# Performance work log

Hardware: AMD Instinct MI355X
Metric: run time of the kernel (lower is better)

Reference implementation:

```python
import jax, jax.numpy as jnp
import numpy as np

KS = 3
N = KS ** 3  # 27 kernel sample points


def conv3d(x, w, b=None, pad=1):
    out = jax.lax.conv_general_dilated(
        x, w, (1, 1, 1), [(pad, pad)] * 3,
        dimension_numbers=('NCDHW', 'OIDHW', 'NCDHW'))
    if b is not None:
        out = out + b[None, :, None, None, None]
    return out


def batchnorm(x, g, b, eps=1e-5):
    # training-mode BN: batch statistics over (N,D,H,W), biased variance (torch default)
    m = x.mean(axis=(0, 2, 3, 4), keepdims=True)
    v = x.var(axis=(0, 2, 3, 4), keepdims=True)
    return (x - m) * jax.lax.rsqrt(v + eps) * g[None, :, None, None, None] + b[None, :, None, None, None]


def deform_conv3d(x, offset, w, pad=1):
    # x: (b,c,D,H,W); offset: (b,3N,D,H,W) channel order [d-offsets | h-offsets | w-offsets]
    b, c, D, H, W = x.shape
    xp = jnp.pad(x, ((0, 0), (0, 0), (pad, pad), (pad, pad), (pad, pad)))
    Dp, Hp, Wp = D + 2 * pad, H + 2 * pad, W + 2 * pad
    dt = offset.dtype
    r = (jnp.arange(KS) - (KS - 1) // 2).astype(dt)
    pn = jnp.stack(jnp.meshgrid(r, r, r, indexing='ij'), -1).reshape(N, 3)  # kernel grid offsets
    base = jnp.stack(jnp.meshgrid(jnp.arange(D) + pad, jnp.arange(H) + pad,
                                  jnp.arange(W) + pad, indexing='ij'), -1).astype(dt)  # (D,H,W,3)
    off = jnp.transpose(offset.reshape(b, 3, N, D, H, W), (0, 3, 4, 5, 2, 1))  # (b,D,H,W,N,3)
    p = base[None, :, :, :, None, :] + pn[None, None, None, None] + off  # fractional sample coords
    dims = jnp.array([Dp, Hp, Wp], dtype=dt)
    q0 = jnp.floor(p)
    q0c = jnp.clip(q0, 0, dims - 1)
    q1c = jnp.clip(q0 + 1, 0, dims - 1)
    pc = jnp.clip(p, 0, dims - 1)
    wlo = 1.0 + (q0c - pc)  # per-axis trilinear weight, low corner
    whi = 1.0 - (q1c - pc)  # per-axis trilinear weight, high corner
    q0i = q0c.astype(jnp.int32)
    q1i = q1c.astype(jnp.int32)
    xpf = xp.reshape(b, c, -1)
    M = D * H * W * N
    acc = jnp.zeros((b, c, D, H, W, N), dtype=x.dtype)
    for corner in range(8):  # fixed 8 trilinear corners
        sel = [(corner >> a) & 1 for a in range(3)]
        q = [q1i[..., a] if sel[a] else q0i[..., a] for a in range(3)]
        g = (whi[..., 0] if sel[0] else wlo[..., 0]) \
            * (whi[..., 1] if sel[1] else wlo[..., 1]) \
            * (whi[..., 2] if sel[2] else wlo[..., 2])
        idx = (q[0] * Hp + q[1]) * Wp + q[2]  # (b,D,H,W,N) flat gather index
        vals = jnp.take_along_axis(
            xpf, jnp.broadcast_to(idx.reshape(b, 1, M), (b, c, M)), axis=2
        ).reshape(b, c, D, H, W, N)
        acc = acc + g[:, None] * vals
    # kernel-stride-KS conv over the reshaped blocks == contraction over (c, N)
    outc = w.shape[0]
    return jnp.einsum('bcdhwn,ocn->bodhw', acc, w.reshape(outc, c, N))


def setup_inputs():
    key = jax.random.key(0)
    ks = jax.random.split(key, 8)
    f32 = jnp.float32
    return {
        'x': jax.random.normal(ks[0], (16, 1, 28, 28, 28), f32),
        'off_w': jax.random.normal(ks[1], (81, 1, 3, 3, 3), f32) * 0.05,
        'off_b': jnp.zeros((81,), f32),
        'dconv_w': jax.random.normal(ks[2], (32, 1, 3, 3, 3), f32) * 0.2,
        'bn1_g': jnp.ones((32,), f32), 'bn1_b': jnp.zeros((32,), f32),
        'conv2_w': jax.random.normal(ks[3], (64, 32, 3, 3, 3), f32) * 0.06,
        'conv2_b': jnp.zeros((64,), f32),
        'bn2_g': jnp.ones((64,), f32), 'bn2_b': jnp.zeros((64,), f32),
        'conv3_w': jax.random.normal(ks[4], (128, 64, 3, 3, 3), f32) * 0.04,
        'conv3_b': jnp.zeros((128,), f32),
        'bn3_g': jnp.ones((128,), f32), 'bn3_b': jnp.zeros((128,), f32),
        'conv4_w': jax.random.normal(ks[5], (128, 128, 3, 3, 3), f32) * 0.03,
        'conv4_b': jnp.zeros((128,), f32),
        'bn4_g': jnp.ones((128,), f32), 'bn4_b': jnp.zeros((128,), f32),
        'fc_w': jax.random.normal(ks[6], (10, 128), f32) * 0.1,
        'fc_b': jnp.zeros((10,), f32),
    }


def reference(x, off_w, off_b, dconv_w, bn1_g, bn1_b, conv2_w, conv2_b, bn2_g, bn2_b,
              conv3_w, conv3_b, bn3_g, bn3_b, conv4_w, conv4_b, bn4_g, bn4_b, fc_w, fc_b):
    offsets = conv3d(x, off_w, off_b)  # (b,81,D,H,W)
    h = batchnorm(jax.nn.relu(deform_conv3d(x, offsets, dconv_w)), bn1_g, bn1_b)
    h = batchnorm(jax.nn.relu(conv3d(h, conv2_w, conv2_b)), bn2_g, bn2_b)
    h = batchnorm(jax.nn.relu(conv3d(h, conv3_w, conv3_b)), bn3_g, bn3_b)
    h = batchnorm(jax.nn.relu(conv3d(h, conv4_w, conv4_b)), bn4_g, bn4_b)
    h = h.mean(axis=(2, 3, 4))  # avg_pool3d over full (28,28,d) -> (b,128)
    logits = h @ fc_w.T + fc_b
    return jax.nn.log_softmax(logits, axis=1), offsets
```

## Files before the change

kernel.cpp:

```cpp
#include <hip/hip_runtime.h>
#include <math.h>

#define Sv 21952
#define HWc 784
#define CNT 351232.0f
#define EPS 1e-5f
#define PV 27000
#define PT (16 * PV)

typedef short bf16x8 __attribute__((ext_vector_type(8)));
typedef float f32x4 __attribute__((ext_vector_type(4)));
typedef float f32x16 __attribute__((ext_vector_type(16)));
typedef unsigned short u16x8 __attribute__((ext_vector_type(8)));

__device__ __forceinline__ unsigned short f2bf(float f) {
    unsigned u = __float_as_uint(f);
    u = (u + 0x7FFFu + ((u >> 16) & 1u)) >> 16;
    return (unsigned short)u;
}
__device__ __forceinline__ float bf2f(unsigned short h) {
    return __uint_as_float(((unsigned)h) << 16);
}

__device__ __forceinline__ void async16(const unsigned short* g, unsigned short* l) {
    __builtin_amdgcn_global_load_lds(
        (const __attribute__((address_space(1))) unsigned int*)g,
        (__attribute__((address_space(3))) unsigned int*)l, 16, 0, 0);
}

template<int C>
__global__ __launch_bounds__(256) void k_zborder(unsigned short* __restrict__ buf) {
    int idx = blockIdx.x * 256 + threadIdx.x;
    if (idx >= PT) return;
    int p = idx % PV;
    int z = p / 900, y = (p / 30) % 30, x = p % 30;
    if (z >= 1 && z <= 28 && y >= 1 && y <= 28 && x >= 1 && x <= 28) return;
    u16x8 zv = {0, 0, 0, 0, 0, 0, 0, 0};
    u16x8* dst = (u16x8*)(buf + (long)idx * C);
    #pragma unroll
    for (int q = 0; q < C / 8; q++) dst[q] = zv;
}

__global__ __launch_bounds__(256) void k_offsets(const float* __restrict__ x,
        const float* __restrict__ ow, const float* __restrict__ ob,
        float* __restrict__ out) {
    int idx = blockIdx.x * 256 + threadIdx.x;
    int n = idx / Sv, s = idx % Sv;
    int d = s / HWc, r = s % HWc, h = r / 28, w = r % 28;
    const float* xb = x + (long)n * Sv;
    float xv[27];
    #pragma unroll
    for (int dz = 0; dz < 3; dz++)
      #pragma unroll
      for (int dy = 0; dy < 3; dy++)
        #pragma unroll
        for (int dx = 0; dx < 3; dx++) {
            int zz = d + dz - 1, yy = h + dy - 1, xx = w + dx - 1;
            bool ok = (unsigned)zz < 28u && (unsigned)yy < 28u && (unsigned)xx < 28u;
            xv[dz * 9 + dy * 3 + dx] = ok ? xb[zz * HWc + yy * 28 + xx] : 0.f;
        }
    float* op = out + (long)n * 81 * Sv + s;
    for (int c = 0; c < 81; c++) {
        float acc = ob[c];
        #pragma unroll
        for (int k = 0; k < 27; k++) acc += xv[k] * ow[c * 27 + k];
        op[(long)c * Sv] = acc;
    }
}

__device__ __forceinline__ float fetch_pad(const float* __restrict__ xb,
                                           int zq, int yq, int xq) {
    int z = zq - 1, y = yq - 1, xx = xq - 1;
    bool ok = (unsigned)z < 28u && (unsigned)y < 28u && (unsigned)xx < 28u;
    return ok ? xb[z * HWc + y * 28 + xx] : 0.f;
}

__global__ __launch_bounds__(256) void k_deform(const float* __restrict__ x,
        const float* __restrict__ off, const float* __restrict__ dw,
        unsigned short* __restrict__ h1p) {
    __shared__ float w_s[32 * 27];
    for (int i = threadIdx.x; i < 32 * 27; i += 256) w_s[i] = dw[i];
    __syncthreads();
    int idx = blockIdx.x * 256 + threadIdx.x;
    int n = idx / Sv, s = idx % Sv;
    int d = s / HWc, r = s % HWc, h = r / 28, w = r % 28;
    const float* xb = x + (long)n * Sv;
    const float* ofb = off + (long)n * 81 * Sv + s;
    float v[27];
    #pragma unroll
    for (int k = 0; k < 27; k++) {
        int ki = k / 9, kj = (k / 3) % 3, kl = k % 3;
        float pd = (float)(d + ki) + ofb[(long)k * Sv];
        float ph = (float)(h + kj) + ofb[(long)(27 + k) * Sv];
        float pw = (float)(w + kl) + ofb[(long)(54 + k) * Sv];
        float q0d = floorf(pd), q0h = floorf(ph), q0w = floorf(pw);
        float pcd = fminf(fmaxf(pd, 0.f), 29.f);
        float pch = fminf(fmaxf(ph, 0.f), 29.f);
        float pcw = fminf(fmaxf(pw, 0.f), 29.f);
        float q0cd = fminf(fmaxf(q0d, 0.f), 29.f);
        float q0ch = fminf(fmaxf(q0h, 0.f), 29.f);
        float q0cw = fminf(fmaxf(q0w, 0.f), 29.f);
        float q1cd = fminf(fmaxf(q0d + 1.f, 0.f), 29.f);
        float q1ch = fminf(fmaxf(q0h + 1.f, 0.f), 29.f);
        float q1cw = fminf(fmaxf(q0w + 1.f, 0.f), 29.f);
        float wz[2] = {1.f + (q0cd - pcd), 1.f - (q1cd - pcd)};
        float wy[2] = {1.f + (q0ch - pch), 1.f - (q1ch - pch)};
        float wx[2] = {1.f + (q0cw - pcw), 1.f - (q1cw - pcw)};
        int qz[2] = {(int)q0cd, (int)q1cd};
        int qy[2] = {(int)q0ch, (int)q1ch};
        int qx[2] = {(int)q0cw, (int)q1cw};
        float val = 0.f;
        #pragma unroll
        for (int cz = 0; cz < 2; cz++)
          #pragma unroll
          for (int cy = 0; cy < 2; cy++)
            #pragma unroll
            for (int cx = 0; cx < 2; cx++)
                val += wz[cz] * wy[cy] * wx[cx] * fetch_pad(xb, qz[cz], qy[cy], qx[cx]);
        v[k] = val;
    }
    unsigned pb = ((((unsigned)n * 30 + (d + 1)) * 30 + (h + 1)) * 30 + (w + 1)) * 32;
    unsigned short tmp[32];
    #pragma unroll
    for (int o = 0; o < 32; o++) {
        float acc = 0.f;
        #pragma unroll
        for (int k = 0; k < 27; k++) acc += v[k] * w_s[o * 27 + k];
        tmp[o] = f2bf(fmaxf(acc, 0.f));
    }
    u16x8* dst = (u16x8*)(h1p + pb);
    #pragma unroll
    for (int q = 0; q < 4; q++) dst[q] = ((u16x8*)tmp)[q];
}

template<int C>
__global__ __launch_bounds__(256) void k_stats_p(const unsigned short* __restrict__ buf,
        float* __restrict__ sums) {
    constexpr int G = C / 8;
    constexpr int P = 256 / G;
    int t = threadIdx.x;
    int oct = t % G, ps = t / G;
    float s1[8], s2[8];
    #pragma unroll
    for (int j = 0; j < 8; j++) { s1[j] = 0.f; s2[j] = 0.f; }
    for (int p = blockIdx.x * P + ps; p < PT; p += gridDim.x * P) {
        u16x8 v = *(const u16x8*)(buf + (long)p * C + oct * 8);
        #pragma unroll
        for (int j = 0; j < 8; j++) {
            float f = bf2f(v[j]);
            s1[j] += f; s2[j] += f * f;
        }
    }
    __shared__ float sh[2][C];
    if (t < C) { sh[0][t] = 0.f; sh[1][t] = 0.f; }
    __syncthreads();
    #pragma unroll
    for (int j = 0; j < 8; j++) {
        atomicAdd(&sh[0][oct * 8 + j], s1[j]);
        atomicAdd(&sh[1][oct * 8 + j], s2[j]);
    }
    __syncthreads();
    if (t < C) { atomicAdd(&sums[t], sh[0][t]); atomicAdd(&sums[C + t], sh[1][t]); }
}

__global__ void k_finalize(const float* __restrict__ sums, const float* __restrict__ g,
        const float* __restrict__ bb, float* __restrict__ aff, int C) {
    int c = threadIdx.x;
    if (c < C) {
        float mean = sums[c] * (1.f / CNT);
        float var = sums[C + c] * (1.f / CNT) - mean * mean;
        float a = g[c] * rsqrtf(var + EPS);
        aff[c] = a;
        aff[C + c] = bb[c] - mean * a;
    }
}

template<int CI, int COT>
__global__ __launch_bounds__(256) void k_wfrag32(const float* __restrict__ w,
        const float* __restrict__ affa, unsigned short* __restrict__ wf) {
    constexpr int NT32 = COT / 32;
    constexpr int KC = CI / 32;
    int tid = blockIdx.x * 256 + threadIdx.x;
    int lane = tid & 63, rest = tid >> 6;
    int kh = rest & 1; rest >>= 1;
    int nt = rest % NT32; rest /= NT32;
    int kc = rest % KC;
    int tap = rest / KC;
    if (tap >= 27) return;
    int co = nt * 32 + (lane & 31);
    int hi = lane >> 5;
    unsigned short tmp[8];
    #pragma unroll
    for (int j = 0; j < 8; j++) {
        int ci = kc * 32 + kh * 16 + hi * 8 + j;
        tmp[j] = f2bf(w[((long)co * CI + ci) * 27 + tap] * affa[ci]);
    }
    long oidx = ((((long)kc * 27 + tap) * NT32 + nt) * 2 + kh) * 512 + lane * 8;
    *(u16x8*)(wf + oidx) = *(u16x8*)tmp;
}

template<int CI, int COT>
__global__ __launch_bounds__(256) void k_tapsum(const float* __restrict__ w,
        const float* __restrict__ affb, float* __restrict__ S) {
    __shared__ float acc[27];
    int co = blockIdx.x;
    int t = threadIdx.x;
    if (t < 27) acc[t] = 0.f;
    __syncthreads();
    const float* wr = w + (long)co * CI * 27;
    for (int idx = t; idx < CI * 27; idx += 256)
        atomicAdd(&acc[idx % 27], wr[idx] * affb[idx / 27]);
    __syncthreads();
    if (t < 27) S[t * COT + co] = acc[t];
}

template<int COT>
__global__ void k_btab2(const float* __restrict__ S, const float* __restrict__ bias,
        float* __restrict__ T) {
    int tid = blockIdx.x * 256 + threadIdx.x;
    if (tid >= 27 * COT) return;
    int co = tid % COT, cls = tid / COT;
    int xc = cls % 3, yc = (cls / 3) % 3, zc = cls / 9;
    float val = bias[co];
    #pragma unroll
    for (int t = 0; t < 27; t++) {
        int dx = t % 3, dy = (t / 3) % 3, dz = t / 9;
        bool ok = (zc == 1 || (zc == 0 && dz >= 1) || (zc == 2 && dz <= 1))
               && (yc == 1 || (yc == 0 && dy >= 1) || (yc == 2 && dy <= 1))
               && (xc == 1 || (xc == 0 && dx >= 1) || (xc == 2 && dx <= 1));
        if (ok) val += S[t * COT + co];
    }
    T[cls * COT + co] = val;
}

template<int CI, int COT, int WN, bool PAD_OUT, int SMODE>
__global__ __launch_bounds__(WN * 128, 2) void k_conv_mfma(
        const unsigned short* __restrict__ in,
        const unsigned short* __restrict__ wfrag,
        const float* __restrict__ Ttab,
        unsigned short* __restrict__ out,
        float* __restrict__ sa, float* __restrict__ sb) {
    constexpr int KC = CI / 32;
    constexpr int NT32 = COT / 32;
    constexpr int NTW = NT32 / 2;
    constexpr int NT = WN * 128;
    constexpr int CP = 720;
    constexpr int CUU = CP * 5;
    constexpr int NLOAD = (CUU + NT - 1) / NT;
    constexpr int LDSU = CUU + 48;
    __shared__ unsigned short lds[LDSU * 8];
    __shared__ float shs[2][COT];

    int tid = threadIdx.x, wv = tid >> 6, lane = tid & 63;
    int lcol = lane & 31, hi = lane >> 5;
    int wv_m = wv & 1, wv_n = wv >> 1;
    if (tid < COT) { shs[0][tid] = 0.f; shs[1][tid] = 0.f; }

    int bx = blockIdx.x;
    int xcd = bx & 7, loc = bx >> 3;
    int n = xcd * 2 + loc / 98;
    int rem = loc % 98;
    int z0 = (rem / 7) * 2;
    int y0 = (rem % 7) * 4;
    const unsigned short* src = in + ((long)((n * 30 + z0) * 30 + y0) * 30) * CI;

    int baseA[4];
    #pragma unroll
    for (int mt = 0; mt < 4; mt++) {
        int x = lcol; if (x > 27) x = 27;
        int pos = (wv_m * 6 + mt) * 30 + x;
        baseA[mt] = pos * 80 + hi * 16;
    }

    f32x16 acc[4][NTW];
    #pragma unroll
    for (int mt = 0; mt < 4; mt++)
        #pragma unroll
        for (int nt = 0; nt < NTW; nt++)
            #pragma unroll
            for (int e = 0; e < 16; e++) acc[mt][nt][e] = 0.f;

    for (int kc = 0; kc < KC; kc++) {
        if (kc) __syncthreads();
        #pragma unroll
        for (int j = 0; j < NLOAD; j++) {
            int wb = j * NT + (wv << 6);
            if (wb < CUU) {
                int u = wb + lane;
                if (u >= CUU) u = CUU - 1;
                int p = u / 5, s = u - p * 5;
                int q = s & 3;
                int zl = p / 180, r = p - zl * 180;
                int yl = r / 30, xl = r - yl * 30;
                int so = (zl * 900 + yl * 30 + xl) * CI + q * 8 + kc * 32;
                async16(src + so, lds + (wb << 3));
            }
        }
        __syncthreads();
        const unsigned short* pwk =
            wfrag + (long)(kc * 27) * NT32 * 1024 + (long)wv_n * (NTW * 1024)
                  + lane * 8;
        bf16x8 bc[NTW][2];
        #pragma unroll
        for (int nt = 0; nt < NTW; nt++)
            #pragma unroll
            for (int kh = 0; kh < 2; kh++)
                bc[nt][kh] = *(const bf16x8*)(pwk + nt * 1024 + kh * 512);
        #pragma unroll
        for (int tap = 0; tap < 27; tap++) {
            int td = (((tap / 9) * 6 + (tap % 9) / 3) * 30 + tap % 3) * 80;
            bf16x8 bn[NTW][2];
            if (tap < 26) {
                const unsigned short* pwn = pwk + (long)(tap + 1) * NT32 * 1024;
                #pragma unroll
                for (int nt = 0; nt < NTW; nt++)
                    #pragma unroll
                    for (int kh = 0; kh < 2; kh++)
                        bn[nt][kh] = *(const bf16x8*)(pwn + nt * 1024 + kh * 512);
            }
            bf16x8 a[2][4];
            #pragma unroll
            for (int kh = 0; kh < 2; kh++)
                #pragma unroll
                for (int mt = 0; mt < 4; mt++)
                    a[kh][mt] = *(const bf16x8*)((const char*)lds
                                 + baseA[mt] + td + kh * 32);
            #pragma unroll
            for (int kh = 0; kh < 2; kh++)
                #pragma unroll
                for (int mt = 0; mt < 4; mt++)
                    #pragma unroll
                    for (int nt = 0; nt < NTW; nt++)
                        acc[mt][nt] = __builtin_amdgcn_mfma_f32_32x32x16_bf16(
                            a[kh][mt], bc[nt][kh], acc[mt][nt], 0, 0, 0);
            if (tap < 26) {
                #pragma unroll
                for (int nt = 0; nt < NTW; nt++)
                    #pragma unroll
                    for (int kh = 0; kh < 2; kh++)
                        bc[nt][kh] = bn[nt][kh];
            }
        }
    }

    int zz = z0 + wv_m;
    int zc = (zz == 0) ? 0 : ((zz == 27) ? 2 : 1);
    float s1a[NTW], s2a[NTW];
    #pragma unroll
    for (int nt = 0; nt < NTW; nt++) { s1a[nt] = 0.f; s2a[nt] = 0.f; }
    #pragma unroll
    for (int mt = 0; mt < 4; mt++) {
        int y = y0 + mt;
        int yc = (y == 0) ? 0 : ((y == 27) ? 2 : 1);
        #pragma unroll
        for (int reg = 0; reg < 16; reg++) {
            int x = (reg & 3) + 8 * (reg >> 2) + 4 * hi;
            if (x >= 28) continue;
            int xc = (x == 0) ? 0 : ((x == 27) ? 2 : 1);
            int cls = (zc * 3 + yc) * 3 + xc;
            long ob = 0;
            if constexpr (SMODE == 0) {
                if (PAD_OUT)
                    ob = ((long)((n * 30 + zz + 1) * 30 + y + 1) * 30 + x + 1) * COT;
                else
                    ob = ((long)n * Sv + zz * HWc + y * 28 + x) * COT;
            }
            #pragma unroll
            for (int nt = 0; nt < NTW; nt++) {
                int co = wv_n * (NTW * 32) + nt * 32 + lcol;
                float v = acc[mt][nt][reg] + Ttab[cls * COT + co];
                unsigned short hb = f2bf(fmaxf(v, 0.f));
                if constexpr (SMODE == 0) out[ob + co] = hb;
                float vr = bf2f(hb);
                s1a[nt] += vr;
                s2a[nt] += vr * vr;
            }
        }
    }
    #pragma unroll
    for (int nt = 0; nt < NTW; nt++) {
        int co = wv_n * (NTW * 32) + nt * 32 + lcol;
        atomicAdd(&shs[0][co], s1a[nt]);
        atomicAdd(&shs[1][co], s2a[nt]);
    }
    __syncthreads();
    if (tid < COT) {
        if constexpr (SMODE == 1) {
            atomicAdd(&sa[n * COT + tid], shs[0][tid]);
        } else {
            atomicAdd(&sa[tid], shs[0][tid]);
        }
        atomicAdd(&sb[tid], shs[1][tid]);
    }
}

__global__ __launch_bounds__(256) void k_head(const float* __restrict__ pooled,
        const float* __restrict__ chsq, const float* __restrict__ g4,
        const float* __restrict__ b4, const float* __restrict__ fcw,
        const float* __restrict__ fcb, float* __restrict__ out) {
    __shared__ float feat[16 * 128];
    __shared__ float lg[160];
    __shared__ float corr[16];
    int t = threadIdx.x;
    if (t < 128) {
        float sum = 0.f;
        for (int n = 0; n < 16; n++) sum += pooled[n * 128 + t];
        float mean = sum * (1.f / CNT);
        float var = chsq[t] * (1.f / CNT) - mean * mean;
        float a = g4[t] * rsqrtf(var + EPS);
        float bb = b4[t] - mean * a;
        for (int n = 0; n < 16; n++)
            feat[n * 128 + t] = a * (pooled[n * 128 + t] * (1.f / (float)Sv)) + bb;
    }
    __syncthreads();
    if (t < 160) {
        int n = t / 10, j = t % 10;
        float acc = fcb[j];
        for (int c = 0; c < 128; c++) acc += feat[n * 128 + c] * fcw[j * 128 + c];
        lg[t] = acc;
    }
    __syncthreads();
    if (t < 16) {
        float mx = -1e30f;
        for (int j = 0; j < 10; j++) mx = fmaxf(mx, lg[t * 10 + j]);
        float se = 0.f;
        for (int j = 0; j < 10; j++) se += expf(lg[t * 10 + j] - mx);
        corr[t] = mx + logf(se);
    }
    __syncthreads();
    if (t < 160) out[t] = lg[t] - corr[t / 10];
}

#define OFF_H3P 0L
#define OFF_H2P 110592000L
#define OFF_H1P 165888000L
#define OFF_WF2 200507392L
#define OFF_WF3 200617984L
#define OFF_WF4 201060352L
#define OFF_STATS 201945088L

extern "C" void kernel_launch(void* const* d_in, const int* in_sizes, int n_in,
                              void* d_out, int out_size, void* d_ws, size_t ws_size,
                              hipStream_t stream) {
    const float* x       = (const float*)d_in[0];
    const float* off_w   = (const float*)d_in[1];
    const float* off_b   = (const float*)d_in[2];
    const float* dconv_w = (const float*)d_in[3];
    const float* bn1_g   = (const float*)d_in[4];
    const float* bn1_b   = (const float*)d_in[5];
    const float* conv2_w = (const float*)d_in[6];
    const float* conv2_b = (const float*)d_in[7];
    const float* bn2_g   = (const float*)d_in[8];
    const float* bn2_b   = (const float*)d_in[9];
    const float* conv3_w = (const float*)d_in[10];
    const float* conv3_b = (const float*)d_in[11];
    const float* bn3_g   = (const float*)d_in[12];
    const float* bn3_b   = (const float*)d_in[13];
    const float* conv4_w = (const float*)d_in[14];
    const float* conv4_b = (const float*)d_in[15];
    const float* bn4_g   = (const float*)d_in[16];
    const float* bn4_b   = (const float*)d_in[17];
    const float* fc_w    = (const float*)d_in[18];
    const float* fc_b    = (const float*)d_in[19];

    float* out = (float*)d_out;
    float* offsets = out + 160;

    char* ws = (char*)d_ws;
    unsigned short* h3p = (unsigned short*)(ws + OFF_H3P);
    unsigned short* h2p = (unsigned short*)(ws + OFF_H2P);
    unsigned short* h1p = (unsigned short*)(ws + OFF_H1P);
    unsigned short* wf2 = (unsigned short*)(ws + OFF_WF2);
    unsigned short* wf3 = (unsigned short*)(ws + OFF_WF3);
    unsigned short* wf4 = (unsigned short*)(ws + OFF_WF4);
    float* st = (float*)(ws + OFF_STATS);
    float* sums1 = st;        float* aff1 = st + 64;
    float* sums2 = st + 128;  float* aff2 = st + 256;
    float* sums3 = st + 384;  float* aff3 = st + 640;
    float* chsq4 = st + 896;  float* pooled = st + 1024;
    float* T2 = st + 4096;    float* T3 = st + 8192;   float* T4 = st + 16384;
    float* Sb = st + 20480;

    hipMemsetAsync(st, 0, 3072 * sizeof(float), stream);
    k_zborder<32><<<dim3(1688), 256, 0, stream>>>(h1p);
    k_zborder<64><<<dim3(1688), 256, 0, stream>>>(h2p);
    k_zborder<128><<<dim3(1688), 256, 0, stream>>>(h3p);

    k_offsets<<<dim3(1372), 256, 0, stream>>>(x, off_w, off_b, offsets);
    k_deform<<<dim3(1372), 256, 0, stream>>>(x, offsets, dconv_w, h1p);

    k_stats_p<32><<<dim3(432), 256, 0, stream>>>(h1p, sums1);
    k_finalize<<<1, 32, 0, stream>>>(sums1, bn1_g, bn1_b, aff1, 32);
    k_wfrag32<32, 64><<<dim3(27), 256, 0, stream>>>(conv2_w, aff1, wf2);
    k_tapsum<32, 64><<<dim3(64), 256, 0, stream>>>(conv2_w, aff1 + 32, Sb);
    k_btab2<64><<<dim3(7), 256, 0, stream>>>(Sb, conv2_b, T2);
    k_conv_mfma<32, 64, 2, true, 0><<<dim3(1568), 256, 0, stream>>>(
        h1p, wf2, T2, h2p, sums2, sums2 + 64);

    k_finalize<<<1, 64, 0, stream>>>(sums2, bn2_g, bn2_b, aff2, 64);
    k_wfrag32<64, 128><<<dim3(108), 256, 0, stream>>>(conv3_w, aff2, wf3);
    k_tapsum<64, 128><<<dim3(128), 256, 0, stream>>>(conv3_w, aff2 + 64, Sb);
    k_btab2<128><<<dim3(14), 256, 0, stream>>>(Sb, conv3_b, T3);
    k_conv_mfma<64, 128, 2, true, 0><<<dim3(1568), 256, 0, stream>>>(
        h2p, wf3, T3, h3p, sums3, sums3 + 128);

    k_finalize<<<1, 128, 0, stream>>>(sums3, bn3_g, bn3_b, aff3, 128);
    k_wfrag32<128, 128><<<dim3(216), 256, 0, stream>>>(conv4_w, aff3, wf4);
    k_tapsum<128, 128><<<dim3(128), 256, 0, stream>>>(conv4_w, aff3 + 128, Sb);
    k_btab2<128><<<dim3(14), 256, 0, stream>>>(Sb, conv4_b, T4);
    k_conv_mfma<128, 128, 2, false, 1><<<dim3(1568), 256, 0, stream>>>(
        h3p, wf4, T4, (unsigned short*)0, pooled, chsq4);

    k_head<<<1, 256, 0, stream>>>(pooled, chsq4, bn4_g, bn4_b, fc_w, fc_b, out);
}
```

Measured before the change: 1.054 ms.

## Split deformable conv kernel taps across two thread halves with LDS reduction

The deformable conv kernel now launches 512 threads per block. Each voxel's 27 trilinear-sampled taps are split between two threads by even and odd index, and each thread computes a partial 32-channel output. The upper half writes its partials to a padded shared array, and after a barrier the lower half adds them and stores bf16 output. This aims to cut per-thread register pressure and the serial gather chain to gain more parallelism, at the cost of 33KB of shared memory per block, a barrier, and half the threads idling during the final store.

```diff
diff --git a/kernel.cpp b/kernel.cpp
--- a/kernel.cpp
+++ b/kernel.cpp
@@ -75,20 +75,25 @@
     return ok ? xb[z * HWc + y * 28 + xx] : 0.f;
 }
 
-__global__ __launch_bounds__(256) void k_deform(const float* __restrict__ x,
+__global__ __launch_bounds__(512) void k_deform(const float* __restrict__ x,
         const float* __restrict__ off, const float* __restrict__ dw,
         unsigned short* __restrict__ h1p) {
     __shared__ float w_s[32 * 27];
-    for (int i = threadIdx.x; i < 32 * 27; i += 256) w_s[i] = dw[i];
-    __syncthreads();
-    int idx = blockIdx.x * 256 + threadIdx.x;
+    __shared__ float part[256][33];
+    for (int i = threadIdx.x; i < 32 * 27; i += 512) w_s[i] = dw[i];
+    __syncthreads();
+    int half = threadIdx.x >> 8;
+    int t = threadIdx.x & 255;
+    int idx = blockIdx.x * 256 + t;
     int n = idx / Sv, s = idx % Sv;
     int d = s / HWc, r = s % HWc, h = r / 28, w = r % 28;
     const float* xb = x + (long)n * Sv;
     const float* ofb = off + (long)n * 81 * Sv + s;
-    float v[27];
-    #pragma unroll
-    for (int k = 0; k < 27; k++) {
+    float v[14];
+    #pragma unroll
+    for (int kk = 0; kk < 14; kk++) {
+        int k = kk * 2 + half;
+        if (k >= 27) { v[kk] = 0.f; continue; }
         int ki = k / 9, kj = (k / 3) % 3, kl = k % 3;
         float pd = (float)(d + ki) + ofb[(long)k * Sv];
         float ph = (float)(h + kj) + ofb[(long)(27 + k) * Sv];
@@ -117,20 +122,34 @@
             #pragma unroll
             for (int cx = 0; cx < 2; cx++)
                 val += wz[cz] * wy[cy] * wx[cx] * fetch_pad(xb, qz[cz], qy[cy], qx[cx]);
-        v[k] = val;
-    }
-    unsigned pb = ((((unsigned)n * 30 + (d + 1)) * 30 + (h + 1)) * 30 + (w + 1)) * 32;
-    unsigned short tmp[32];
+        v[kk] = val;
+    }
+    float acc[32];
     #pragma unroll
     for (int o = 0; o < 32; o++) {
-        float acc = 0.f;
-        #pragma unroll
-        for (int k = 0; k < 27; k++) acc += v[k] * w_s[o * 27 + k];
-        tmp[o] = f2bf(fmaxf(acc, 0.f));
-    }
-    u16x8* dst = (u16x8*)(h1p + pb);
-    #pragma unroll
-    for (int q = 0; q < 4; q++) dst[q] = ((u16x8*)tmp)[q];
+        float a = 0.f;
+        #pragma unroll
+        for (int kk = 0; kk < 14; kk++) {
+            int k = kk * 2 + half;
+            if (k < 27) a += v[kk] * w_s[o * 27 + k];
+        }
+        acc[o] = a;
+    }
+    if (half) {
+        #pragma unroll
+        for (int o = 0; o < 32; o++) part[t][o] = acc[o];
+    }
+    __syncthreads();
+    if (!half) {
+        unsigned pb = ((((unsigned)n * 30 + (d + 1)) * 30 + (h + 1)) * 30 + (w + 1)) * 32;
+        unsigned short tmp[32];
+        #pragma unroll
+        for (int o = 0; o < 32; o++)
+            tmp[o] = f2bf(fmaxf(acc[o] + part[t][o], 0.f));
+        u16x8* dst = (u16x8*)(h1p + pb);
+        #pragma unroll
+        for (int q = 0; q < 4; q++) dst[q] = ((u16x8*)tmp)[q];
+    }
 }
 
 template<int C>
@@ -487,7 +506,7 @@
     k_zborder<128><<<dim3(1688), 256, 0, stream>>>(h3p);
 
     k_offsets<<<dim3(1372), 256, 0, stream>>>(x, off_w, off_b, offsets);
-    k_deform<<<dim3(1372), 256, 0, stream>>>(x, offsets, dconv_w, h1p);
+    k_deform<<<dim3(1372), 512, 0, stream>>>(x, offsets, dconv_w, h1p);
 
     k_stats_p<32><<<dim3(432), 256, 0, stream>>>(h1p, sums1);
     k_finalize<<<1, 32, 0, stream>>>(sums1, bn1_g, bn1_b, aff1, 32);
```

Measured after the change: 1.004 ms. -4.7%, faster.
